# Performance work log

Measured on AMD Instinct MI355X. Metric: run time of the kernel, lower is better.

The kernel has to match this reference:

```python
import jax, jax.numpy as jnp
import numpy as np

B, T, I, H = 512, 256, 256, 512


def setup_inputs() -> dict:
    key = jax.random.key(0)
    k1, k2, k3, k4, k5 = jax.random.split(key, 5)
    s = 1.0 / np.sqrt(H)  # torch LSTMCell init scale
    return {
        "x": jax.random.normal(k1, (B, T, I), dtype=jnp.float32),
        "W_ih": jax.random.uniform(k2, (4 * H, I), dtype=jnp.float32, minval=-s, maxval=s),
        "W_hh": jax.random.uniform(k3, (4 * H, H), dtype=jnp.float32, minval=-s, maxval=s),
        "b_ih": jax.random.uniform(k4, (4 * H,), dtype=jnp.float32, minval=-s, maxval=s),
        "b_hh": jax.random.uniform(k5, (4 * H,), dtype=jnp.float32, minval=-s, maxval=s),
    }


def _att_lstm(x, W_ih, W_hh, b_ih, b_hh):
    batch, hidden = x.shape[0], W_hh.shape[1]
    b = b_ih + b_hh  # (4H,)

    def step(carry, xt):
        h, c = carry
        gates = xt @ W_ih.T + h @ W_hh.T + b  # (B, 4H)
        i, f, g, o = jnp.split(gates, 4, axis=-1)  # torch gate order: i, f, g, o
        i = jax.nn.sigmoid(i)
        f = jax.nn.sigmoid(f)
        g = jnp.tanh(g)
        o = jax.nn.sigmoid(o)
        c_new = f * c + i * g
        h_new = o * jnp.tanh(c_new)
        return (h_new, c_new), h_new

    h0 = jnp.zeros((batch, hidden), dtype=x.dtype)
    c0 = jnp.zeros((batch, hidden), dtype=x.dtype)
    (h_last, _), h_seq = jax.lax.scan(step, (h0, c0), jnp.swapaxes(x, 0, 1))
    h_states = jnp.swapaxes(h_seq, 0, 1)  # (B, T, H)

    # attention pooling: plain score normalization (NOT softmax), as in source
    att_score = jnp.einsum("bth,bh->bt", h_states, h_last)  # (B, T)
    att_dist = att_score / jnp.sum(att_score, axis=1, keepdims=True)
    context = jnp.einsum("bt,bth->bh", att_dist, h_states)  # (B, H)
    return context[:, None, :]  # (B, 1, H)


def reference(x, W_ih, W_hh, b_ih, b_hh):
    return _att_lstm(x, W_ih, W_hh, b_ih, b_hh)
```

## Files before the change

### kernel.cpp

```cpp
#include <hip/hip_runtime.h>

#define BATCH 512
#define TT    256
#define II    256
#define HH    512

typedef float f32x4  __attribute__((ext_vector_type(4)));
typedef unsigned u32x4 __attribute__((ext_vector_type(4)));
typedef unsigned short u16x8 __attribute__((ext_vector_type(8)));
typedef short bfrag  __attribute__((ext_vector_type(8)));

__device__ inline unsigned short f2bf(float f) {
    unsigned u = __float_as_uint(f);
    return (unsigned short)((u + 0x7fffu + ((u >> 16) & 1u)) >> 16);
}
__device__ inline float bf2f(unsigned short h) { return __uint_as_float(((unsigned)h) << 16); }

__device__ inline bfrag cvt8(const float* p) {
    float4 a = *(const float4*)p;
    float4 b = *(const float4*)(p + 4);
    u16x8 u;
    u[0]=f2bf(a.x); u[1]=f2bf(a.y); u[2]=f2bf(a.z); u[3]=f2bf(a.w);
    u[4]=f2bf(b.x); u[5]=f2bf(b.y); u[6]=f2bf(b.z); u[7]=f2bf(b.w);
    return __builtin_bit_cast(bfrag, u);
}
__device__ inline bfrag ld8(const unsigned short* p) {
    return __builtin_bit_cast(bfrag, *(const u16x8*)p);
}
__device__ inline float sigm(float x) { return 1.f / (1.f + __expf(-x)); }
__device__ inline float tanh_(float x) {
    float ax = fabsf(x);
    float e  = __expf(-2.f * ax);
    float t  = (1.f - e) / (1.f + e);
    return copysignf(t, x);
}

__global__ __launch_bounds__(256) void cast_x_kernel(const float* __restrict__ x,
                                                     unsigned short* __restrict__ xt) {
    int b  = blockIdx.x >> 2;
    int t0 = (blockIdx.x & 3) * 64;
    int ic = (threadIdx.x & 31) * 8;
    int tq = threadIdx.x >> 5;
#pragma unroll
    for (int p = 0; p < 8; ++p) {
        int t = t0 + tq * 8 + p;
        const float* src = x + ((long)b * TT + t) * II + ic;
        float4 a = *(const float4*)src;
        float4 bb = *(const float4*)(src + 4);
        u16x8 u;
        u[0]=f2bf(a.x); u[1]=f2bf(a.y); u[2]=f2bf(a.z); u[3]=f2bf(a.w);
        u[4]=f2bf(bb.x); u[5]=f2bf(bb.y); u[6]=f2bf(bb.z); u[7]=f2bf(bb.w);
        *(u16x8*)(xt + ((long)t * BATCH + b) * II + ic) = u;
    }
}

__global__ __launch_bounds__(256, 1) void lstm_persist(
    const float* __restrict__ Wih, const float* __restrict__ Whh,
    const float* __restrict__ bih, const float* __restrict__ bhh,
    const unsigned short* __restrict__ xb,
    unsigned short* __restrict__ hs,
    unsigned short* __restrict__ ring,
    unsigned char* __restrict__ flags)
{
    const int tid  = threadIdx.x;
    const int bx   = blockIdx.x;
    const int grp  = bx >> 4;
    const int wg   = bx & 15;
    const int w    = tid >> 6;
    const int lane = tid & 63;
    const int quad = lane >> 4;
    const int ct   = lane & 15;
    const bool lo  = (ct < 8);
    const int rb0  = grp * 32;
    const int hcol = wg * 32 + w * 8 + (ct & 7);

    __shared__ unsigned short sh[32 * 528];
    __shared__ unsigned short wlds[128 * 272];
    __shared__ unsigned short sh2[32 * 32];

    int wrow[2];
    wrow[0] = ((ct >> 3) + 0) * HH + hcol;
    wrow[1] = ((ct >> 3) + 2) * HH + hcol;

    bfrag wih_f[8][2], whh_r[8][2];
#pragma unroll
    for (int kk = 0; kk < 8; ++kk)
#pragma unroll
        for (int nt = 0; nt < 2; ++nt) {
            wih_f[kk][nt] = cvt8(Wih + (long)wrow[nt] * II + kk * 32 + quad * 8);
            whh_r[kk][nt] = cvt8(Whh + (long)wrow[nt] * HH + kk * 32 + quad * 8);
        }

    for (int e = tid * 8; e < 128 * 256; e += 256 * 8) {
        int lc = e >> 8;
        int k  = e & 255;
        int row = (lc >> 5) * HH + wg * 32 + (lc & 31);
        bfrag f = cvt8(Whh + (long)row * HH + 256 + k);
        *(u16x8*)(wlds + lc * 272 + k) = __builtin_bit_cast(u16x8, f);
    }
    __syncthreads();

    const int wl0 = ((((ct >> 3) + 0) * 32 + w * 8 + (ct & 7)) * 272) + quad * 8;
    const int wl1 = ((((ct >> 3) + 2) * 32 + w * 8 + (ct & 7)) * 272) + quad * 8;

    float bb[2];
    bb[0] = bih[wrow[0]] + bhh[wrow[0]];
    bb[1] = bih[wrow[1]] + bhh[wrow[1]];

    float cst[2][4];
#pragma unroll
    for (int mt = 0; mt < 2; ++mt)
#pragma unroll
        for (int r = 0; r < 4; ++r) cst[mt][r] = 0.f;

    f32x4 acc[2][2];
#pragma unroll
    for (int mt = 0; mt < 2; ++mt)
#pragma unroll
        for (int nt = 0; nt < 2; ++nt)
            acc[mt][nt] = (f32x4){bb[nt], bb[nt], bb[nt], bb[nt]};
#pragma unroll
    for (int kk = 0; kk < 8; ++kk)
#pragma unroll
        for (int mt = 0; mt < 2; ++mt) {
            bfrag a = ld8(xb + ((long)0 * BATCH + rb0 + mt * 16 + ct) * II + kk * 32 + quad * 8);
#pragma unroll
            for (int nt = 0; nt < 2; ++nt)
                acc[mt][nt] = __builtin_amdgcn_mfma_f32_16x16x32_bf16(a, wih_f[kk][nt], acc[mt][nt], 0, 0, 0);
        }

    for (int t = 0; t < TT; ++t) {
        if (t > 0) {
            if (tid == 0) {
                const unsigned char* fp = flags + (((long)grp * TT + (t - 1)) << 4);
                u32x4 fv;
                do {
                    asm volatile("global_load_dwordx4 %0, %1, off sc0 sc1\n\ts_waitcnt vmcnt(0)"
                                 : "=v"(fv) : "v"(fp) : "memory");
                } while (fv.x != 0x01010101u || fv.y != 0x01010101u ||
                         fv.z != 0x01010101u || fv.w != 0x01010101u);
            }
            __syncthreads();

            const unsigned short* rbase = ring + (((long)grp * 4 + ((t - 1) & 3)) * 32) * HH;
            u32x4 vv[8];
#pragma unroll
            for (int j = 0; j < 8; ++j) {
                int cid = j * 256 + tid;
                int row = cid >> 6, c16 = cid & 63;
                const unsigned short* p = rbase + row * HH + c16 * 8;
                asm volatile("global_load_dwordx4 %0, %1, off sc0 sc1"
                             : "=v"(vv[j]) : "v"(p));
            }
            asm volatile("s_waitcnt vmcnt(0)" ::: "memory");
#pragma unroll
            for (int j = 0; j < 8; ++j) {
                int cid = j * 256 + tid;
                int row = cid >> 6, c16 = cid & 63;
                *(u32x4*)(sh + row * 528 + c16 * 8) = vv[j];
            }
            __syncthreads();

#pragma unroll
            for (int kk = 0; kk < 8; ++kk) {
                bfrag a[2];
#pragma unroll
                for (int mt = 0; mt < 2; ++mt)
                    a[mt] = ld8(sh + (mt * 16 + ct) * 528 + kk * 32 + quad * 8);
#pragma unroll
                for (int mt = 0; mt < 2; ++mt)
#pragma unroll
                    for (int nt = 0; nt < 2; ++nt)
                        acc[mt][nt] = __builtin_amdgcn_mfma_f32_16x16x32_bf16(a[mt], whh_r[kk][nt], acc[mt][nt], 0, 0, 0);
            }
#pragma unroll
            for (int kk = 0; kk < 8; ++kk) {
                bfrag a[2], b[2];
#pragma unroll
                for (int mt = 0; mt < 2; ++mt)
                    a[mt] = ld8(sh + (mt * 16 + ct) * 528 + (8 + kk) * 32 + quad * 8);
                b[0] = ld8(wlds + wl0 + kk * 32);
                b[1] = ld8(wlds + wl1 + kk * 32);
#pragma unroll
                for (int mt = 0; mt < 2; ++mt)
#pragma unroll
                    for (int nt = 0; nt < 2; ++nt)
                        acc[mt][nt] = __builtin_amdgcn_mfma_f32_16x16x32_bf16(a[mt], b[nt], acc[mt][nt], 0, 0, 0);
            }
        }

#pragma unroll
        for (int mt = 0; mt < 2; ++mt) {
#pragma unroll
            for (int r = 0; r < 4; ++r) {
                float a0 = acc[mt][0][r], a1 = acc[mt][1][r];
                float b0 = __shfl_xor(a0, 8, 64);
                float b1 = __shfl_xor(a1, 8, 64);
                float iv = lo ? a0 : b0;
                float fv = lo ? b0 : a0;
                float gv = lo ? a1 : b1;
                float ov = lo ? b1 : a1;
                iv = sigm(iv); fv = sigm(fv); gv = tanh_(gv); ov = sigm(ov);
                float c = fv * cst[mt][r] + iv * gv;
                cst[mt][r] = c;
                float h = ov * tanh_(c);
                if (lo)
                    sh2[(mt * 16 + quad * 4 + r) * 32 + w * 8 + (ct & 7)] = f2bf(h);
            }
        }
        __syncthreads();

        if (tid < 128) {
            int row = tid >> 2, c = tid & 3;
            u32x4 v = *(const u32x4*)(sh2 + row * 32 + c * 8);
            *(u32x4*)(hs + ((long)(rb0 + row) * TT + t) * HH + wg * 32 + c * 8) = v;
            unsigned short* rp = ring + (((long)grp * 4 + (t & 3)) * 32 + row) * HH + wg * 32 + c * 8;
            asm volatile("global_store_dwordx4 %0, %1, off sc0 sc1"
                         :: "v"(rp), "v"(v) : "memory");
        }

        if (t < TT - 1) {
#pragma unroll
            for (int mt = 0; mt < 2; ++mt)
#pragma unroll
                for (int nt = 0; nt < 2; ++nt)
                    acc[mt][nt] = (f32x4){bb[nt], bb[nt], bb[nt], bb[nt]};
#pragma unroll
            for (int kk = 0; kk < 8; ++kk)
#pragma unroll
                for (int mt = 0; mt < 2; ++mt) {
                    bfrag a = ld8(xb + ((long)(t + 1) * BATCH + rb0 + mt * 16 + ct) * II + kk * 32 + quad * 8);
#pragma unroll
                    for (int nt = 0; nt < 2; ++nt)
                        acc[mt][nt] = __builtin_amdgcn_mfma_f32_16x16x32_bf16(a, wih_f[kk][nt], acc[mt][nt], 0, 0, 0);
                }

            asm volatile("s_waitcnt vmcnt(0)" ::: "memory");
            __syncthreads();
            if (tid == 0) {
                unsigned one = 1u;
                unsigned char* p = flags + ((((long)grp * TT + t) << 4) | wg);
                asm volatile("global_store_byte %0, %1, off sc0 sc1"
                             :: "v"(p), "v"(one) : "memory");
            }
        }
    }
}

__global__ __launch_bounds__(256) void attn_kernel(const unsigned short* __restrict__ hs,
                                                   float* __restrict__ out) {
    int b = blockIdx.x, tid = threadIdx.x;
    int w = tid >> 6, lane = tid & 63;
    __shared__ float sc[TT];
    __shared__ float hl[HH];
    for (int c = tid; c < HH; c += 256)
        hl[c] = bf2f(hs[((long)b * TT + (TT - 1)) * HH + c]);
    __syncthreads();
    float hr[8];
#pragma unroll
    for (int j = 0; j < 8; ++j) hr[j] = hl[lane * 8 + j];
    for (int t = w; t < TT; t += 4) {
        u16x8 hv = *(const u16x8*)(hs + ((long)b * TT + t) * HH + lane * 8);
        float p = 0.f;
#pragma unroll
        for (int j = 0; j < 8; ++j) p += bf2f(hv[j]) * hr[j];
#pragma unroll
        for (int off = 32; off; off >>= 1) p += __shfl_xor(p, off, 64);
        if (lane == 0) sc[t] = p;
    }
    __syncthreads();
    float denom = 0.f;
    for (int t = 0; t < TT; ++t) denom += sc[t];
    float c0 = 0.f, c1 = 0.f;
    int col = tid * 2;
    for (int t = 0; t < TT; ++t) {
        float s = sc[t];
        unsigned v = *(const unsigned*)(hs + ((long)b * TT + t) * HH + col);
        c0 += s * __uint_as_float((v & 0xffffu) << 16);
        c1 += s * __uint_as_float(v & 0xffff0000u);
    }
    out[(long)b * HH + col]     = c0 / denom;
    out[(long)b * HH + col + 1] = c1 / denom;
}

extern "C" void kernel_launch(void* const* d_in, const int* in_sizes, int n_in,
                              void* d_out, int out_size, void* d_ws, size_t ws_size,
                              hipStream_t stream) {
    const float* x   = (const float*)d_in[0];
    const float* Wih = (const float*)d_in[1];
    const float* Whh = (const float*)d_in[2];
    const float* bih = (const float*)d_in[3];
    const float* bhh = (const float*)d_in[4];
    float* out = (float*)d_out;

    char* ws = (char*)d_ws;
    unsigned char*  flags = (unsigned char*)ws;
    unsigned short* ring  = (unsigned short*)(ws + 65536);
    unsigned short* hs    = (unsigned short*)(ws + 65536 + 2097152);
    unsigned short* xb    = (unsigned short*)(ws + 65536 + 2097152 + (size_t)BATCH * TT * HH * 2);

    (void)hipMemsetAsync(flags, 0, 65536, stream);
    cast_x_kernel<<<BATCH * (TT / 64), 256, 0, stream>>>(x, xb);
    lstm_persist<<<256, 256, 0, stream>>>(Wih, Whh, bih, bhh, xb, hs, ring, flags);
    attn_kernel<<<BATCH, 256, 0, stream>>>(hs, out);
}
```

Baseline: 2.010 ms.

## Drop ring buffer, publish per-wave flags right after h stores, remap blocks

```diff
diff --git a/kernel.cpp b/kernel.cpp
--- a/kernel.cpp
+++ b/kernel.cpp
@@ -59,13 +59,12 @@
     const float* __restrict__ bih, const float* __restrict__ bhh,
     const unsigned short* __restrict__ xb,
     unsigned short* __restrict__ hs,
-    unsigned short* __restrict__ ring,
     unsigned char* __restrict__ flags)
 {
     const int tid  = threadIdx.x;
     const int bx   = blockIdx.x;
-    const int grp  = bx >> 4;
-    const int wg   = bx & 15;
+    const int grp  = bx & 15;
+    const int wg   = bx >> 4;
     const int w    = tid >> 6;
     const int lane = tid & 63;
     const int quad = lane >> 4;
@@ -123,7 +122,7 @@
     for (int kk = 0; kk < 8; ++kk)
 #pragma unroll
         for (int mt = 0; mt < 2; ++mt) {
-            bfrag a = ld8(xb + ((long)0 * BATCH + rb0 + mt * 16 + ct) * II + kk * 32 + quad * 8);
+            bfrag a = ld8(xb + ((long)(rb0 + mt * 16 + ct)) * II + kk * 32 + quad * 8);
 #pragma unroll
             for (int nt = 0; nt < 2; ++nt)
                 acc[mt][nt] = __builtin_amdgcn_mfma_f32_16x16x32_bf16(a, wih_f[kk][nt], acc[mt][nt], 0, 0, 0);
@@ -132,30 +131,33 @@
     for (int t = 0; t < TT; ++t) {
         if (t > 0) {
             if (tid == 0) {
-                const unsigned char* fp = flags + (((long)grp * TT + (t - 1)) << 4);
-                u32x4 fv;
+                const unsigned char* fp = flags + (((long)grp * TT + (t - 1)) << 5);
+                u32x4 f0, f1;
                 do {
-                    asm volatile("global_load_dwordx4 %0, %1, off sc0 sc1\n\ts_waitcnt vmcnt(0)"
-                                 : "=v"(fv) : "v"(fp) : "memory");
-                } while (fv.x != 0x01010101u || fv.y != 0x01010101u ||
-                         fv.z != 0x01010101u || fv.w != 0x01010101u);
+                    asm volatile("global_load_dwordx4 %0, %2, off sc0 sc1\n\t"
+                                 "global_load_dwordx4 %1, %2, off offset:16 sc0 sc1\n\t"
+                                 "s_waitcnt vmcnt(0)"
+                                 : "=v"(f0), "=v"(f1) : "v"(fp) : "memory");
+                } while (f0.x != 0x01010101u || f0.y != 0x01010101u ||
+                         f0.z != 0x01010101u || f0.w != 0x01010101u ||
+                         f1.x != 0x01010101u || f1.y != 0x01010101u ||
+                         f1.z != 0x01010101u || f1.w != 0x01010101u);
             }
             __syncthreads();
 
-            const unsigned short* rbase = ring + (((long)grp * 4 + ((t - 1) & 3)) * 32) * HH;
             u32x4 vv[8];
 #pragma unroll
             for (int j = 0; j < 8; ++j) {
-                int cid = j * 256 + tid;
+                int cid = (j * 256 + tid + (wg << 7)) & 2047;
                 int row = cid >> 6, c16 = cid & 63;
-                const unsigned short* p = rbase + row * HH + c16 * 8;
-                asm volatile("global_load_dwordx4 %0, %1, off sc0 sc1"
+                const unsigned short* p = hs + ((long)(rb0 + row) * TT + (t - 1)) * HH + c16 * 8;
+                asm volatile("global_load_dwordx4 %0, %1, off sc0"
                              : "=v"(vv[j]) : "v"(p));
             }
             asm volatile("s_waitcnt vmcnt(0)" ::: "memory");
 #pragma unroll
             for (int j = 0; j < 8; ++j) {
-                int cid = j * 256 + tid;
+                int cid = (j * 256 + tid + (wg << 7)) & 2047;
                 int row = cid >> 6, c16 = cid & 63;
                 *(u32x4*)(sh + row * 528 + c16 * 8) = vv[j];
             }
@@ -213,10 +215,18 @@
         if (tid < 128) {
             int row = tid >> 2, c = tid & 3;
             u32x4 v = *(const u32x4*)(sh2 + row * 32 + c * 8);
-            *(u32x4*)(hs + ((long)(rb0 + row) * TT + t) * HH + wg * 32 + c * 8) = v;
-            unsigned short* rp = ring + (((long)grp * 4 + (t & 3)) * 32 + row) * HH + wg * 32 + c * 8;
+            unsigned short* p = hs + ((long)(rb0 + row) * TT + t) * HH + wg * 32 + c * 8;
             asm volatile("global_store_dwordx4 %0, %1, off sc0 sc1"
-                         :: "v"(rp), "v"(v) : "memory");
+                         :: "v"(p), "v"(v) : "memory");
+            if (t < TT - 1) {
+                asm volatile("s_waitcnt vmcnt(0)" ::: "memory");
+                if ((tid & 63) == 0) {
+                    unsigned one = 1u;
+                    unsigned char* fp2 = flags + ((((long)grp * TT + t) << 5) | (wg * 2 + w));
+                    asm volatile("global_store_byte %0, %1, off sc0 sc1"
+                                 :: "v"(fp2), "v"(one) : "memory");
+                }
+            }
         }
 
         if (t < TT - 1) {
@@ -234,15 +244,6 @@
                     for (int nt = 0; nt < 2; ++nt)
                         acc[mt][nt] = __builtin_amdgcn_mfma_f32_16x16x32_bf16(a, wih_f[kk][nt], acc[mt][nt], 0, 0, 0);
                 }
-
-            asm volatile("s_waitcnt vmcnt(0)" ::: "memory");
-            __syncthreads();
-            if (tid == 0) {
-                unsigned one = 1u;
-                unsigned char* p = flags + ((((long)grp * TT + t) << 4) | wg);
-                asm volatile("global_store_byte %0, %1, off sc0 sc1"
-                             :: "v"(p), "v"(one) : "memory");
-            }
         }
     }
 }
@@ -295,12 +296,11 @@
 
     char* ws = (char*)d_ws;
     unsigned char*  flags = (unsigned char*)ws;
-    unsigned short* ring  = (unsigned short*)(ws + 65536);
-    unsigned short* hs    = (unsigned short*)(ws + 65536 + 2097152);
-    unsigned short* xb    = (unsigned short*)(ws + 65536 + 2097152 + (size_t)BATCH * TT * HH * 2);
-
-    (void)hipMemsetAsync(flags, 0, 65536, stream);
+    unsigned short* hs    = (unsigned short*)(ws + 131072);
+    unsigned short* xb    = (unsigned short*)(ws + 131072 + (size_t)BATCH * TT * HH * 2);
+
+    (void)hipMemsetAsync(flags, 0, 131072, stream);
     cast_x_kernel<<<BATCH * (TT / 64), 256, 0, stream>>>(x, xb);
-    lstm_persist<<<256, 256, 0, stream>>>(Wih, Whh, bih, bhh, xb, hs, ring, flags);
+    lstm_persist<<<256, 256, 0, stream>>>(Wih, Whh, bih, bhh, xb, hs, flags);
     attn_kernel<<<BATCH, 256, 0, stream>>>(hs, out);
 }
```

After: 1.825 ms. -9.2%, faster.
